# Optimization experiments

Hardware: AMD Instinct MI355X
Metric: run time of the kernel (lower is better)

The kernel has to match this reference:

```python
import jax, jax.numpy as jnp
import numpy as np
from jax import lax

NUM_HEADS = 3
HEAD_CH = 64  # in_ch // num_heads = 192 // 3
EPS = 1e-5   # haiku BatchNorm default eps


def _conv_proj(x, dw, scale, offset, pw, stride):
    # DepthwiseConv2D (SAME, no bias) -> BatchNorm (training: batch stats) -> 1x1 Conv (no bias)
    C = x.shape[-1]
    x = lax.conv_general_dilated(
        x, dw, (stride, stride), 'SAME',
        dimension_numbers=('NHWC', 'HWIO', 'NHWC'),
        feature_group_count=C)
    mean = x.mean(axis=(0, 1, 2))
    var = x.var(axis=(0, 1, 2))
    x = (x - mean) * lax.rsqrt(var + EPS) * scale + offset
    return jnp.einsum('bhwc,cd->bhwd', x, pw)  # pointwise 1x1 conv


def _split_heads(x):
    # b H W (h d) -> b h (H W) d
    b, hh, ww, c = x.shape
    return x.reshape(b, hh * ww, NUM_HEADS, HEAD_CH).transpose(0, 2, 1, 3)


def setup_inputs() -> dict:
    key = jax.random.key(0)
    ks = jax.random.split(key, 18)
    B, H, W, C = 16, 56, 56, 192
    Cout = NUM_HEADS * HEAD_CH  # 192
    g = lambda k, shape, s=0.02: jax.random.normal(k, shape, jnp.float32) * s
    return {
        'inputs_q':  jax.random.normal(ks[0], (B, H, W, C), jnp.float32),
        'inputs_kv': jax.random.normal(ks[1], (B, H, W, C), jnp.float32),
        # depthwise kernels (k, k, 1, C)
        'dw_q': g(ks[2], (3, 3, 1, C)), 'dw_k': g(ks[3], (3, 3, 1, C)), 'dw_v': g(ks[4], (3, 3, 1, C)),
        # BN scale/offset per projection
        'scale_q': jnp.ones((C,), jnp.float32), 'offset_q': jnp.zeros((C,), jnp.float32),
        'scale_k': jnp.ones((C,), jnp.float32), 'offset_k': jnp.zeros((C,), jnp.float32),
        'scale_v': jnp.ones((C,), jnp.float32), 'offset_v': jnp.zeros((C,), jnp.float32),
        # pointwise 1x1 conv kernels (C, Cout)
        'pw_q': g(ks[5], (C, Cout)), 'pw_k': g(ks[6], (C, Cout)), 'pw_v': g(ks[7], (C, Cout)),
        # talking-heads mixing matrices (h, h), near-identity init
        'pre_sm':  jnp.eye(NUM_HEADS, dtype=jnp.float32) + g(ks[8], (NUM_HEADS, NUM_HEADS), 0.1),
        'post_sm': jnp.eye(NUM_HEADS, dtype=jnp.float32) + g(ks[9], (NUM_HEADS, NUM_HEADS), 0.1),
        # output linear (no bias)
        'w_out': g(ks[10], (Cout, C)),
    }


def reference(inputs_q, inputs_kv, dw_q, dw_k, dw_v,
              scale_q, offset_q, scale_k, offset_k, scale_v, offset_v,
              pw_q, pw_k, pw_v, pre_sm, post_sm, w_out):
    q = _conv_proj(inputs_q,  dw_q, scale_q, offset_q, pw_q, 1)  # [B,56,56,192]
    k = _conv_proj(inputs_kv, dw_k, scale_k, offset_k, pw_k, 2)  # [B,28,28,192]
    v = _conv_proj(inputs_kv, dw_v, scale_v, offset_v, pw_v, 2)
    B = q.shape[0]
    q = _split_heads(q) / jnp.sqrt(jnp.float32(HEAD_CH))  # [B,h,Lq,d]
    k = _split_heads(k)                                   # [B,h,Lk,d]
    v = _split_heads(v)
    w = jnp.einsum('bhld,bhkd->bhlk', q, k)               # [B,h,Lq,Lk]
    w = jnp.einsum('bhlk,hg->bglk', w, pre_sm)            # pre-softmax talking heads
    w = jax.nn.softmax(w, axis=-1)
    w = jnp.einsum('bhlk,hg->bglk', w, post_sm)           # post-softmax talking heads
    s = jnp.einsum('bhlk,bhkd->bhld', w, v)               # [B,h,Lq,d]
    s = s.transpose(0, 2, 1, 3).reshape(B, -1, NUM_HEADS * HEAD_CH)  # b l (h d)
    return s @ w_out                                      # [B,Lq,192]
```

## Files before the change

kernel.cpp:

```cpp
#include <hip/hip_runtime.h>

using short8 = __attribute__((ext_vector_type(8))) short;
using f32x4  = __attribute__((ext_vector_type(4))) float;

__device__ __forceinline__ short f2bf(float f){
  unsigned u = __float_as_uint(f);
  unsigned r = (u + 0x7FFFu + ((u >> 16) & 1u)) >> 16;
  return (short)r;
}
__device__ __forceinline__ float sget(float x){
  return __uint_as_float(__builtin_amdgcn_readfirstlane(__float_as_uint(x)));
}
__device__ __forceinline__ unsigned cvtpk_bf16(float lo, float hi){
  unsigned d;
  asm("v_cvt_pk_bf16_f32 %0, %1, %2" : "=v"(d) : "v"(lo), "v"(hi));
  return d;
}
__device__ __forceinline__ void async_cp16(short* lds, const short* g){
  __builtin_amdgcn_global_load_lds((const __attribute__((address_space(1))) unsigned int*)g,
                                   (__attribute__((address_space(3))) unsigned int*)lds,
                                   16, 0, 0);
}

__global__ __launch_bounds__(384) void k_dw(const float* __restrict__ inq, const float* __restrict__ inkv,
                                            const float* __restrict__ wq, const float* __restrict__ wk,
                                            const float* __restrict__ wv,
                                            short* __restrict__ dqb, short* __restrict__ dkb,
                                            short* __restrict__ dvb, float2* __restrict__ partq,
                                            float2* __restrict__ partk, float2* __restrict__ partv){
  __shared__ float red[4][384];
  int t = threadIdx.x;
  int c = t % 192, strip = t / 192;
  if(blockIdx.x < 896){
    int bid = blockIdx.x; int b = bid / 56, oh = bid % 56;
    float w[9];
#pragma unroll
    for(int i=0;i<9;i++) w[i] = wq[i*192 + c];
    const float* inb = inq + (size_t)b*56*56*192;
    const float* rp[3]; bool rv[3];
#pragma unroll
    for(int kh=0;kh<3;kh++){
      int ih = oh + kh - 1;
      rv[kh] = (ih >= 0 && ih < 56);
      rp[kh] = inb + (size_t)(rv[kh] ? ih : 0)*56*192 + c;
    }
    auto ldc = [&](int kh, int iw)->float{
      return (rv[kh] && iw >= 0 && iw < 56) ? rp[kh][iw*192] : 0.f;
    };
    int ow0 = strip*28;
    float x0[3], x1[3];
#pragma unroll
    for(int kh=0;kh<3;kh++){ x0[kh] = ldc(kh, ow0-1); x1[kh] = ldc(kh, ow0); }
    float lsum = 0.f, lsq = 0.f;
    size_t orow = ((size_t)b*3136 + (size_t)oh*56)*192;
#pragma unroll 1
    for(int j=0;j<28;j++){
      int ow = ow0 + j;
      float x2[3];
#pragma unroll
      for(int kh=0;kh<3;kh++) x2[kh] = ldc(kh, ow+1);
      float acc = 0.f;
#pragma unroll
      for(int kh=0;kh<3;kh++){
        acc = fmaf(x0[kh], w[kh*3+0], acc);
        acc = fmaf(x1[kh], w[kh*3+1], acc);
        acc = fmaf(x2[kh], w[kh*3+2], acc);
      }
      dqb[orow + (size_t)ow*192 + c] = f2bf(acc);
      lsum += acc; lsq = fmaf(acc, acc, lsq);
#pragma unroll
      for(int kh=0;kh<3;kh++){ x0[kh] = x1[kh]; x1[kh] = x2[kh]; }
    }
    red[0][t] = lsum; red[1][t] = lsq;
    __syncthreads();
    if(t < 192){
      float2 o; o.x = lsum + red[0][t+192]; o.y = lsq + red[1][t+192];
      partq[(size_t)bid*192 + t] = o;
    }
  } else {
    int bid = blockIdx.x - 896; int b = bid / 28, oh = bid % 28;
    float wkr[9], wvr[9];
#pragma unroll
    for(int i=0;i<9;i++){ wkr[i] = wk[i*192 + c]; wvr[i] = wv[i*192 + c]; }
    const float* inb = inkv + (size_t)b*56*56*192;
    const float* rp[3]; bool rv[3];
#pragma unroll
    for(int kh=0;kh<3;kh++){
      int ih = 2*oh + kh;
      rv[kh] = (ih < 56);
      rp[kh] = inb + (size_t)(rv[kh] ? ih : 0)*56*192 + c;
    }
    auto ldc = [&](int kh, int iw)->float{
      return (rv[kh] && iw < 56) ? rp[kh][iw*192] : 0.f;
    };
    int ow0 = strip*14;
    float xp[3];
#pragma unroll
    for(int kh=0;kh<3;kh++) xp[kh] = ldc(kh, 2*ow0);
    float ksum=0.f, ksq=0.f, vsum=0.f, vsq=0.f;
    size_t orow = ((size_t)b*784 + (size_t)oh*28)*192;
#pragma unroll 1
    for(int j=0;j<14;j++){
      int ow = ow0 + j;
      float xm[3], xn[3];
#pragma unroll
      for(int kh=0;kh<3;kh++){ xm[kh] = ldc(kh, 2*ow+1); xn[kh] = ldc(kh, 2*ow+2); }
      float ak = 0.f, av = 0.f;
#pragma unroll
      for(int kh=0;kh<3;kh++){
        ak = fmaf(xp[kh], wkr[kh*3+0], ak); ak = fmaf(xm[kh], wkr[kh*3+1], ak); ak = fmaf(xn[kh], wkr[kh*3+2], ak);
        av = fmaf(xp[kh], wvr[kh*3+0], av); av = fmaf(xm[kh], wvr[kh*3+1], av); av = fmaf(xn[kh], wvr[kh*3+2], av);
      }
      dkb[orow + (size_t)ow*192 + c] = f2bf(ak);
      dvb[orow + (size_t)ow*192 + c] = f2bf(av);
      ksum += ak; ksq = fmaf(ak, ak, ksq);
      vsum += av; vsq = fmaf(av, av, vsq);
#pragma unroll
      for(int kh=0;kh<3;kh++) xp[kh] = xn[kh];
    }
    red[0][t]=ksum; red[1][t]=ksq; red[2][t]=vsum; red[3][t]=vsq;
    __syncthreads();
    if(t < 192){
      float2 a; a.x = ksum + red[0][t+192]; a.y = ksq + red[1][t+192];
      partk[(size_t)bid*192 + t] = a;
      float2 o; o.x = vsum + red[2][t+192]; o.y = vsq + red[3][t+192];
      partv[(size_t)bid*192 + t] = o;
    }
  }
}

__global__ __launch_bounds__(192) void k_red(const float2* __restrict__ pq, const float2* __restrict__ pk,
                                             const float2* __restrict__ pv, float2* __restrict__ oq,
                                             float2* __restrict__ ok2, float2* __restrict__ ov2){
  int blk = blockIdx.x, t = threadIdx.x;
  const float2* src; float2* dst;
  if(blk < 8){ src = pq + (size_t)blk*112*192;      dst = oq  + (size_t)blk*192; }
  else if(blk < 12){ src = pk + (size_t)(blk-8)*112*192;  dst = ok2 + (size_t)(blk-8)*192; }
  else { src = pv + (size_t)(blk-12)*112*192; dst = ov2 + (size_t)(blk-12)*192; }
  float s=0.f, q=0.f;
#pragma unroll 8
  for(int i=0;i<112;i++){ float2 v = src[(size_t)i*192 + t]; s += v.x; q += v.y; }
  float2 o; o.x=s; o.y=q; dst[t] = o;
}

__global__ __launch_bounds__(192) void k_fin(const float2* __restrict__ pq, const float2* __restrict__ pk,
                                             const float2* __restrict__ pv,
                                             const float* __restrict__ sq, const float* __restrict__ oq,
                                             const float* __restrict__ sk, const float* __restrict__ ok,
                                             const float* __restrict__ sv, const float* __restrict__ ov,
                                             const float* __restrict__ pwq, const float* __restrict__ pwk,
                                             const float* __restrict__ pwv, const float* __restrict__ wout,
                                             short* __restrict__ Wt, float* __restrict__ bias){
  int p = blockIdx.x, t = threadIdx.x;
  __shared__ float aS[192], bS[192];
  if(p < 3){
    const float2* part = (p==0)?pq:((p==1)?pk:pv);
    int nb = (p==0)?8:4;
    float N = (p==0)?50176.f:12544.f;
    const float* sc = (p==0)?sq:((p==1)?sk:sv);
    const float* of = (p==0)?oq:((p==1)?ok:ov);
    float s=0.f, q2=0.f;
#pragma unroll
    for(int i=0;i<8;i++){ if(i<nb){ float2 v = part[(size_t)i*192 + t]; s += v.x; q2 += v.y; } }
    float mean = s / N;
    float var  = q2 / N - mean*mean;
    float a  = rsqrtf(var + 1e-5f) * sc[t];
    float bv = of[t] - mean*a;
    aS[t] = a; bS[t] = bv;
    __syncthreads();
    const float* pw = (p==0)?pwq:((p==1)?pwk:pwv);
    float qs = (p==0) ? 0.125f : 1.0f;
    float bacc = 0.f;
    for(int cc=0; cc<192; cc++){
      float wv_ = pw[cc*192 + t];
      bacc = fmaf(bS[cc], wv_, bacc);
      Wt[((size_t)p*192 + t)*192 + cc] = f2bf(aS[cc]*wv_*qs);
    }
    bias[p*192 + t] = bacc * qs;
  } else {
    for(int cc=0; cc<192; cc++) Wt[((size_t)3*192 + t)*192 + cc] = f2bf(wout[cc*192 + t]);
    bias[3*192 + t] = 0.f;
  }
}

__global__ __launch_bounds__(256) void k_kv(const short* __restrict__ dkb, const short* __restrict__ dvb,
                                            const short* __restrict__ Wt, const float* __restrict__ bias,
                                            short* __restrict__ kbuf, short* __restrict__ vtb){
  int blk = blockIdx.x;
  bool isV = blk >= 208;
  int pb = isV ? blk - 208 : blk;
  int w = threadIdx.x >> 6, L = threadIdx.x & 63, l16 = L & 15, h4 = L >> 4;
  int row0 = pb*64 + w*16;
  int b = row0 / 832, kk0 = row0 - b*832;
  const short* A = isV ? dvb : dkb;
  const short* Wp = Wt + (isV ? 2 : 1)*36864;
  const float* bp = bias + (isV ? 2 : 1)*192;
  int kkA = kk0 + l16; if(kkA > 783) kkA = 783;
  short8 af[6];
  const short8* arow = (const short8*)(A + (size_t)(b*784 + kkA)*192);
#pragma unroll
  for(int kf=0;kf<6;kf++) af[kf] = arow[kf*4 + h4];
  short* obase = (isV ? vtb : kbuf) + (size_t)b*26*6144;
#pragma unroll
  for(int nt=0;nt<12;nt++){
    f32x4 acc = f32x4{0.f,0.f,0.f,0.f};
    const short8* wrow = (const short8*)(Wp + (size_t)(nt*16 + l16)*192);
#pragma unroll
    for(int kf=0;kf<6;kf++)
      acc = __builtin_amdgcn_mfma_f32_16x16x32_bf16(af[kf], wrow[kf*4 + h4], acc, 0,0,0);
    int col = nt*16 + l16;
    float bv = bp[col];
#pragma unroll
    for(int r=0;r<4;r++){
      int kk = kk0 + h4*4 + r;
      float v = (kk < 784) ? (acc[r] + bv) : 0.f;
      int t = kk >> 5, rr = kk & 31;
      if(!isV) obase[(size_t)t*6144 + (col>>3)*256 + rr*8 + (col&7)] = f2bf(v);
      else     obase[(size_t)t*6144 + (rr>>3)*1536 + col*8 + (rr&7)] = f2bf(v);
    }
  }
}

__global__ __launch_bounds__(256, 2) void k_attn(const short* __restrict__ dq, const short* __restrict__ Wt,
                                                 const float* __restrict__ bias,
                                                 const short* __restrict__ kb, const short* __restrict__ vt,
                                                 const float* __restrict__ pre, const float* __restrict__ post,
                                                 float* __restrict__ outp){
  __shared__ __align__(16) short sS[38400];
  short* sKb = sS;
  short* sVb = sS + 12288;
  short* sP  = sS + 30720;
  int bid = blockIdx.x;
  int b  = ((bid & 7) << 1) | ((bid >> 3) & 1);
  int lt = bid >> 4;
  int tid = threadIdx.x; int w = tid >> 6, lane = tid & 63, l16 = lane & 15, h4 = lane >> 4;
  int lw = lt*64 + w*16;
  short* sScr = sS + w*3200;

  {
    short8 af[6];
    const short8* arow = (const short8*)(dq + ((size_t)b*3136 + lw + l16)*192);
#pragma unroll
    for(int kf=0;kf<6;kf++) af[kf] = arow[kf*4 + h4];
#pragma unroll
    for(int nt=0;nt<12;nt++){
      f32x4 acc = f32x4{0.f,0.f,0.f,0.f};
      const short8* wrow = (const short8*)(Wt + (size_t)(nt*16 + l16)*192);
#pragma unroll
      for(int kf=0;kf<6;kf++)
        acc = __builtin_amdgcn_mfma_f32_16x16x32_bf16(af[kf], wrow[kf*4 + h4], acc, 0,0,0);
      float bv = bias[nt*16 + l16];
#pragma unroll
      for(int r=0;r<4;r++) sScr[(h4*4+r)*200 + nt*16 + l16] = f2bf(acc[r] + bv);
    }
  }
  short8 qf[3][2];
#pragma unroll
  for(int h=0;h<3;h++)
#pragma unroll
    for(int kf=0;kf<2;kf++) qf[h][kf] = *(const short8*)&sScr[l16*200 + h*64 + kf*32 + h4*8];

  float pm[3][3];
#pragma unroll
  for(int h=0;h<3;h++)
#pragma unroll
    for(int g=0;g<3;g++) pm[h][g] = sget(pre[h*3+g]) * 1.44269504f;

  f32x4 T[3][3][4];
#pragma unroll
  for(int g=0;g<3;g++)
#pragma unroll
    for(int gp=0;gp<3;gp++)
#pragma unroll
      for(int nt=0;nt<4;nt++) T[g][gp][nt] = f32x4{0.f,0.f,0.f,0.f};
  float Zp[3] = {0.f, 0.f, 0.f};

  const short* kgb = kb + (size_t)b*26*6144;
  const short* vgb = vt + (size_t)b*26*6144;
  int soff = w*1536;

  auto stage = [&](int t){
    short* kl = sKb + (t&1)*6144 + soff;
    short* vl = sVb + (t%3)*6144 + soff;
    const short* kg = kgb + (size_t)t*6144 + soff + lane*8;
    const short* vg = vgb + (size_t)t*6144 + soff + lane*8;
#pragma unroll
    for(int j=0;j<3;j++){
      async_cp16(kl + j*512, kg + j*512);
      async_cp16(vl + j*512, vg + j*512);
    }
  };

  __syncthreads();
  stage(0);
  __syncthreads();

  int sPw = w*1920;
#pragma unroll 1
  for(int ks=0; ks<25; ks++){
    if(ks < 24) stage(ks+1);
    const short* sKc = sKb + (ks&1)*6144;
    f32x4 acc[3][2];
#pragma unroll
    for(int h=0;h<3;h++)
#pragma unroll
      for(int nt=0;nt<2;nt++) acc[h][nt] = f32x4{0.f,0.f,0.f,0.f};
#pragma unroll
    for(int h=0;h<3;h++)
#pragma unroll
      for(int kf=0;kf<2;kf++){
        short8 aq = qf[h][kf];
#pragma unroll
        for(int nt=0;nt<2;nt++){
          short8 bk = *(const short8*)&sKc[(h*8 + kf*4 + h4)*256 + (nt*16 + l16)*8];
          acc[h][nt] = __builtin_amdgcn_mfma_f32_16x16x32_bf16(bk, aq, acc[h][nt], 0,0,0);
        }
      }
    if(ks){
      const short* sVp = sVb + ((ks-1)%3)*6144 + h4*1536;
      short8 pa[3];
#pragma unroll
      for(int g=0;g<3;g++) pa[g] = *(const short8*)&sP[sPw + g*640 + l16*40 + h4*8];
#pragma unroll
      for(int gp=0;gp<3;gp++)
#pragma unroll
        for(int nt=0;nt<4;nt++){
          short8 vb = *(const short8*)(sVp + (gp*64 + nt*16 + l16)*8);
#pragma unroll
          for(int g=0;g<3;g++)
            T[g][gp][nt] = __builtin_amdgcn_mfma_f32_16x16x32_bf16(pa[g], vb, T[g][gp][nt], 0,0,0);
        }
    }
#pragma unroll
    for(int nt=0;nt<2;nt++){
      bool zok = (ks < 24) || (nt == 0);
#pragma unroll
      for(int g=0;g<3;g++){
        float e[4];
#pragma unroll
        for(int r=0;r<4;r++){
          float sm = fmaf(pm[0][g], acc[0][nt][r], fmaf(pm[1][g], acc[1][nt][r], pm[2][g]*acc[2][nt][r]));
          e[r] = exp2f(sm);
        }
        if(zok) Zp[g] += (e[0] + e[1]) + (e[2] + e[3]);
        uint2 dw; dw.x = cvtpk_bf16(e[0], e[1]); dw.y = cvtpk_bf16(e[2], e[3]);
        *(uint2*)&sP[sPw + g*640 + l16*40 + nt*16 + h4*4] = dw;
      }
    }
    __syncthreads();
  }
  {
    const short* sVp = sVb + (24%3)*6144 + h4*1536;
    short8 pa[3];
#pragma unroll
    for(int g=0;g<3;g++) pa[g] = *(const short8*)&sP[sPw + g*640 + l16*40 + h4*8];
#pragma unroll
    for(int gp=0;gp<3;gp++)
#pragma unroll
      for(int nt=0;nt<4;nt++){
        short8 vb = *(const short8*)(sVp + (gp*64 + nt*16 + l16)*8);
#pragma unroll
        for(int g=0;g<3;g++)
          T[g][gp][nt] = __builtin_amdgcn_mfma_f32_16x16x32_bf16(pa[g], vb, T[g][gp][nt], 0,0,0);
      }
  }

  float izq[3][4];
#pragma unroll
  for(int g=0;g<3;g++){
    float z = Zp[g];
    z += __shfl_xor(z, 16); z += __shfl_xor(z, 32);
    float iz = 1.f / z;
#pragma unroll
    for(int r=0;r<4;r++) izq[g][r] = __shfl(iz, h4*4 + r);
  }
  float po[3][3];
#pragma unroll
  for(int g=0;g<3;g++)
#pragma unroll
    for(int gp=0;gp<3;gp++) po[g][gp] = sget(post[g*3+gp]);

#pragma unroll
  for(int gp=0;gp<3;gp++){
    float cg[3][4];
#pragma unroll
    for(int g=0;g<3;g++)
#pragma unroll
      for(int r=0;r<4;r++) cg[g][r] = po[g][gp] * izq[g][r];
#pragma unroll
    for(int nt=0;nt<4;nt++){
#pragma unroll
      for(int r=0;r<4;r++){
        float u = fmaf(cg[0][r], T[0][gp][nt][r], fmaf(cg[1][r], T[1][gp][nt][r], cg[2][r]*T[2][gp][nt][r]));
        sScr[(h4*4+r)*200 + gp*64 + nt*16 + l16] = f2bf(u);
      }
    }
  }
  short8 uf[6];
#pragma unroll
  for(int kf=0;kf<6;kf++) uf[kf] = *(const short8*)&sScr[l16*200 + kf*32 + h4*8];
  const short* W3 = Wt + 3*36864;
#pragma unroll
  for(int nt=0;nt<12;nt++){
    f32x4 acc = f32x4{0.f,0.f,0.f,0.f};
    const short8* wrow = (const short8*)(W3 + (size_t)(nt*16 + l16)*192);
#pragma unroll
    for(int kf=0;kf<6;kf++)
      acc = __builtin_amdgcn_mfma_f32_16x16x32_bf16(uf[kf], wrow[kf*4 + h4], acc, 0,0,0);
#pragma unroll
    for(int r=0;r<4;r++)
      outp[((size_t)b*3136 + lw + h4*4 + r)*192 + nt*16 + l16] = acc[r];
  }
}

extern "C" void kernel_launch(void* const* d_in, const int* in_sizes, int n_in,
                              void* d_out, int out_size, void* d_ws, size_t ws_size,
                              hipStream_t stream){
  (void)in_sizes; (void)n_in; (void)out_size; (void)ws_size;
  const float* inq  = (const float*)d_in[0];
  const float* inkv = (const float*)d_in[1];
  const float* dwq  = (const float*)d_in[2];
  const float* dwk  = (const float*)d_in[3];
  const float* dwv  = (const float*)d_in[4];
  const float* scq  = (const float*)d_in[5];  const float* ofq = (const float*)d_in[6];
  const float* sck  = (const float*)d_in[7];  const float* ofk = (const float*)d_in[8];
  const float* scv  = (const float*)d_in[9];  const float* ofv = (const float*)d_in[10];
  const float* pwq  = (const float*)d_in[11];
  const float* pwk  = (const float*)d_in[12];
  const float* pwv  = (const float*)d_in[13];
  const float* pre  = (const float*)d_in[14];
  const float* post = (const float*)d_in[15];
  const float* wout = (const float*)d_in[16];

  char* ws = (char*)d_ws;
  size_t off = 0;
  auto alloc = [&](size_t bytes)->void*{ void* p = ws + off; off += (bytes + 255) & ~(size_t)255; return p; };
  short*  dqb  = (short*) alloc(50176ull*192*2);
  short*  dkb  = (short*) alloc(12544ull*192*2);
  short*  dvb  = (short*) alloc(12544ull*192*2);
  short*  kbuf = (short*) alloc(16ull*26*6144*2);
  short*  vtb  = (short*) alloc(16ull*26*6144*2);
  float2* pq   = (float2*)alloc(896ull*192*sizeof(float2));
  float2* pk   = (float2*)alloc(448ull*192*sizeof(float2));
  float2* pv   = (float2*)alloc(448ull*192*sizeof(float2));
  float2* pq2  = (float2*)alloc(8ull*192*sizeof(float2));
  float2* pk2  = (float2*)alloc(4ull*192*sizeof(float2));
  float2* pv2  = (float2*)alloc(4ull*192*sizeof(float2));
  short*  Wt   = (short*) alloc(4ull*192*192*2);
  float*  bias = (float*) alloc(4ull*192*4);

  k_dw<<<1344, 384, 0, stream>>>(inq, inkv, dwq, dwk, dwv, dqb, dkb, dvb, pq, pk, pv);
  k_red<<<16, 192, 0, stream>>>(pq, pk, pv, pq2, pk2, pv2);
  k_fin<<<4, 192, 0, stream>>>(pq2, pk2, pv2, scq, ofq, sck, ofk, scv, ofv, pwq, pwk, pwv, wout, Wt, bias);
  k_kv<<<416, 256, 0, stream>>>(dkb, dvb, Wt, bias, kbuf, vtb);
  k_attn<<<784, 256, 0, stream>>>(dqb, Wt, bias, kbuf, vtb, pre, post, (float*)d_out);
}
```

Before: 234.3 us.

## Unskew PV pipeline: consume P in same iteration, double-buffer V, add setprio

The attention loop previously computed P for tile ks and ran the PV MFMAs one iteration later, which needed a triple-buffered V ring in LDS. It now computes QK and softmax per 16-column subtile, writes P, and immediately multiplies by the V tile staged for the same step. That lets V use a double buffer and shrinks LDS, and s_setprio marks the MFMA sections so waves can interleave. The cost is less overlap between the exp/softmax and the PV MFMAs within a wave, and the P written to LDS is read back by the same wave with no sync in between.

```diff
diff --git a/kernel.cpp b/kernel.cpp
--- a/kernel.cpp
+++ b/kernel.cpp
@@ -226,10 +226,10 @@
                                                  const short* __restrict__ kb, const short* __restrict__ vt,
                                                  const float* __restrict__ pre, const float* __restrict__ post,
                                                  float* __restrict__ outp){
-  __shared__ __align__(16) short sS[38400];
+  __shared__ __align__(16) short sS[32256];
   short* sKb = sS;
   short* sVb = sS + 12288;
-  short* sP  = sS + 30720;
+  short* sP  = sS + 24576;
   int bid = blockIdx.x;
   int b  = ((bid & 7) << 1) | ((bid >> 3) & 1);
   int lt = bid >> 4;
@@ -281,7 +281,7 @@
 
   auto stage = [&](int t){
     short* kl = sKb + (t&1)*6144 + soff;
-    short* vl = sVb + (t%3)*6144 + soff;
+    short* vl = sVb + (t&1)*6144 + soff;
     const short* kg = kgb + (size_t)t*6144 + soff + lane*8;
     const short* vg = vgb + (size_t)t*6144 + soff + lane*8;
 #pragma unroll
@@ -300,46 +300,28 @@
   for(int ks=0; ks<25; ks++){
     if(ks < 24) stage(ks+1);
     const short* sKc = sKb + (ks&1)*6144;
-    f32x4 acc[3][2];
-#pragma unroll
-    for(int h=0;h<3;h++)
-#pragma unroll
-      for(int nt=0;nt<2;nt++) acc[h][nt] = f32x4{0.f,0.f,0.f,0.f};
-#pragma unroll
-    for(int h=0;h<3;h++)
-#pragma unroll
-      for(int kf=0;kf<2;kf++){
-        short8 aq = qf[h][kf];
-#pragma unroll
-        for(int nt=0;nt<2;nt++){
+    const short* sVc = sVb + (ks&1)*6144;
+#pragma unroll
+    for(int nt=0;nt<2;nt++){
+      f32x4 a3[3];
+#pragma unroll
+      for(int h=0;h<3;h++) a3[h] = f32x4{0.f,0.f,0.f,0.f};
+      __builtin_amdgcn_s_setprio(1);
+#pragma unroll
+      for(int h=0;h<3;h++)
+#pragma unroll
+        for(int kf=0;kf<2;kf++){
           short8 bk = *(const short8*)&sKc[(h*8 + kf*4 + h4)*256 + (nt*16 + l16)*8];
-          acc[h][nt] = __builtin_amdgcn_mfma_f32_16x16x32_bf16(bk, aq, acc[h][nt], 0,0,0);
+          a3[h] = __builtin_amdgcn_mfma_f32_16x16x32_bf16(bk, qf[h][kf], a3[h], 0,0,0);
         }
-      }
-    if(ks){
-      const short* sVp = sVb + ((ks-1)%3)*6144 + h4*1536;
-      short8 pa[3];
-#pragma unroll
-      for(int g=0;g<3;g++) pa[g] = *(const short8*)&sP[sPw + g*640 + l16*40 + h4*8];
-#pragma unroll
-      for(int gp=0;gp<3;gp++)
-#pragma unroll
-        for(int nt=0;nt<4;nt++){
-          short8 vb = *(const short8*)(sVp + (gp*64 + nt*16 + l16)*8);
-#pragma unroll
-          for(int g=0;g<3;g++)
-            T[g][gp][nt] = __builtin_amdgcn_mfma_f32_16x16x32_bf16(pa[g], vb, T[g][gp][nt], 0,0,0);
-        }
-    }
-#pragma unroll
-    for(int nt=0;nt<2;nt++){
+      __builtin_amdgcn_s_setprio(0);
       bool zok = (ks < 24) || (nt == 0);
 #pragma unroll
       for(int g=0;g<3;g++){
         float e[4];
 #pragma unroll
         for(int r=0;r<4;r++){
-          float sm = fmaf(pm[0][g], acc[0][nt][r], fmaf(pm[1][g], acc[1][nt][r], pm[2][g]*acc[2][nt][r]));
+          float sm = fmaf(pm[0][g], a3[0][r], fmaf(pm[1][g], a3[1][r], pm[2][g]*a3[2][r]));
           e[r] = exp2f(sm);
         }
         if(zok) Zp[g] += (e[0] + e[1]) + (e[2] + e[3]);
@@ -347,22 +329,21 @@
         *(uint2*)&sP[sPw + g*640 + l16*40 + nt*16 + h4*4] = dw;
       }
     }
-    __syncthreads();
-  }
-  {
-    const short* sVp = sVb + (24%3)*6144 + h4*1536;
     short8 pa[3];
 #pragma unroll
     for(int g=0;g<3;g++) pa[g] = *(const short8*)&sP[sPw + g*640 + l16*40 + h4*8];
+    __builtin_amdgcn_s_setprio(1);
 #pragma unroll
     for(int gp=0;gp<3;gp++)
 #pragma unroll
       for(int nt=0;nt<4;nt++){
-        short8 vb = *(const short8*)(sVp + (gp*64 + nt*16 + l16)*8);
+        short8 vb = *(const short8*)&sVc[h4*1536 + (gp*64 + nt*16 + l16)*8];
 #pragma unroll
         for(int g=0;g<3;g++)
           T[g][gp][nt] = __builtin_amdgcn_mfma_f32_16x16x32_bf16(pa[g], vb, T[g][gp][nt], 0,0,0);
       }
+    __builtin_amdgcn_s_setprio(0);
+    __syncthreads();
   }
 
   float izq[3][4];
```

New measurement: 238.4 us. About the same (+1.7%).
